# Optimization experiments

Measured on AMD Instinct MI355X. Metric: run time of the kernel, lower is better.

## Reference

```python
import jax, jax.numpy as jnp
import numpy as np

NUM_HEADS = 12
SIZE_PER_HEAD = 64
NEG_INF = -10000.0


def setup_inputs() -> dict:
    key = jax.random.key(0)
    k1, k2, k3, k4 = jax.random.split(key, 4)
    B, S, D = 2, 2048, 768
    x = jax.random.normal(k1, (B, S, D), dtype=jnp.float32)
    mask = jax.random.randint(k2, (B, S, S), 0, 2, dtype=jnp.int32)
    std = 0.02
    Wq = jax.random.normal(k3, (D, NUM_HEADS * SIZE_PER_HEAD), dtype=jnp.float32) * std
    Wk = jax.random.normal(k4, (D, NUM_HEADS * SIZE_PER_HEAD), dtype=jnp.float32) * std
    bq = jnp.zeros((NUM_HEADS * SIZE_PER_HEAD,), dtype=jnp.float32)
    bk = jnp.zeros((NUM_HEADS * SIZE_PER_HEAD,), dtype=jnp.float32)
    return {"x": x, "mask": mask, "Wq": Wq, "bq": bq, "Wk": Wk, "bk": bk}


def reference(x, mask, Wq, bq, Wk, bk):
    B, S, D = x.shape
    H, dh = NUM_HEADS, SIZE_PER_HEAD
    # Dense query/key projections (no activation), then split heads: [B,H,S,dh]
    q = (x @ Wq + bq).reshape(B, S, H, dh).transpose(0, 2, 1, 3)
    k = (x @ Wk + bk).reshape(B, S, H, dh).transpose(0, 2, 1, 3)
    # Scaled dot-product scores: [B,H,S,S]
    scores = jnp.einsum("bhqd,bhkd->bhqk", q, k) / jnp.sqrt(jnp.float32(dh))
    # Mask: [B,S,S] -> [B,1,S,S]; zeros get large negative additive bias
    adder = (1.0 - mask.astype(jnp.float32))[:, None, :, :] * NEG_INF
    probs = jax.nn.softmax(scores + adder, axis=-1)
    # dropout is identity at inference (training=None)
    return probs
```

## Files before the change

### kernel.cpp

```cpp
#include <hip/hip_runtime.h>
#include <stdint.h>

#define NUM_HEADS 12
#define DH 64
#define SEQ 2048
#define BATCH 2
#define DM 768
#define NQK 1536
#define LOG2E 1.44269504088896340736f

typedef short short8 __attribute__((ext_vector_type(8)));
typedef short short4_t __attribute__((ext_vector_type(4)));
typedef float f32x4 __attribute__((ext_vector_type(4)));

__device__ __forceinline__ short bf16_rne(float f) {
    union { float f; uint32_t u; } v; v.f = f;
    return (short)((v.u + 0x7FFFu + ((v.u >> 16) & 1u)) >> 16);
}

__global__ __launch_bounds__(256) void prep_kernel(const float* __restrict__ Wq,
                                                   const float* __restrict__ Wk,
                                                   const float* __restrict__ x,
                                                   const int* __restrict__ mask,
                                                   short* __restrict__ Wt,
                                                   short* __restrict__ Xb,
                                                   unsigned long long* __restrict__ Mb) {
    __shared__ float tile[32][33];
    const int bid = blockIdx.x;
    const int t = threadIdx.x;
    if (bid < 1152) {
        int n0 = (bid % 48) * 32;
        int k0 = (bid / 48) * 32;
        int tx = t & 31;
        int ty = t >> 5;
        const float* src = (n0 < DM) ? Wq : Wk;
        int nn0 = (n0 < DM) ? n0 : n0 - DM;
#pragma unroll
        for (int j = 0; j < 4; ++j) {
            int k = ty + 8 * j;
            tile[k][tx] = src[(size_t)(k0 + k) * DM + nn0 + tx];
        }
        __syncthreads();
#pragma unroll
        for (int j = 0; j < 4; ++j) {
            int n = ty + 8 * j;
            Wt[(size_t)(n0 + n) * DM + k0 + tx] = bf16_rne(tile[tx][n]);
        }
    } else if (bid < 1920) {
        size_t base = (size_t)(bid - 1152) * 4096;
#pragma unroll
        for (int j = 0; j < 4; ++j) {
            size_t i = base + (size_t)(t + j * 256) * 4;
            f32x4 v = *(const f32x4*)(x + i);
            short4_t s;
#pragma unroll
            for (int e = 0; e < 4; ++e) s[e] = bf16_rne(v[e]);
            *(short4_t*)(Xb + i) = s;
        }
    } else {
        int wid = (bid - 1920) * 4 + (t >> 6);
        int lane = t & 63;
        size_t base = (size_t)wid * 8;
#pragma unroll
        for (int i = 0; i < 8; ++i) {
            size_t w = base + i;
            int v = mask[w * 64 + lane];
            unsigned long long bal = __ballot(v != 0);
            if (lane == 0) Mb[w] = bal;
        }
    }
}

__global__ __launch_bounds__(256) void proj_kernel(const short* __restrict__ Xb,
                                                   const short* __restrict__ Wt,
                                                   const float* __restrict__ bq,
                                                   const float* __restrict__ bk,
                                                   short* __restrict__ QK) {
    __shared__ short As[128 * 72];
    __shared__ short Bs[128 * 72];
    const int m0 = blockIdx.x * 128;
    const int n0 = blockIdx.y * 128;
    const int t = threadIdx.x;
    const int lane = t & 63;
    const int w = t >> 6;
    const int wr = w >> 1, wc = w & 1;
    const int lr = lane & 15;
    const int lk = lane >> 4;

    f32x4 acc[4][4] = {};

    for (int k0 = 0; k0 < DM; k0 += 64) {
#pragma unroll
        for (int j = 0; j < 4; ++j) {
            int idx = t + 256 * j;
            int row = idx >> 3;
            int ch = idx & 7;
            *(short8*)&As[row * 72 + ch * 8] =
                *(const short8*)&Xb[(size_t)(m0 + row) * DM + k0 + ch * 8];
            *(short8*)&Bs[row * 72 + ch * 8] =
                *(const short8*)&Wt[(size_t)(n0 + row) * DM + k0 + ch * 8];
        }
        __syncthreads();
#pragma unroll
        for (int kk = 0; kk < 2; ++kk) {
            short8 a[4], bfr[4];
#pragma unroll
            for (int m = 0; m < 4; ++m)
                a[m] = *(short8*)&As[(wr * 64 + m * 16 + lr) * 72 + kk * 32 + lk * 8];
#pragma unroll
            for (int n = 0; n < 4; ++n)
                bfr[n] = *(short8*)&Bs[(wc * 64 + n * 16 + lr) * 72 + kk * 32 + lk * 8];
#pragma unroll
            for (int m = 0; m < 4; ++m)
#pragma unroll
                for (int n = 0; n < 4; ++n)
                    acc[m][n] = __builtin_amdgcn_mfma_f32_16x16x32_bf16(a[m], bfr[n], acc[m][n], 0, 0, 0);
        }
        __syncthreads();
    }

    const int orow = m0 + wr * 64;
    const int ocol = n0 + wc * 64;
#pragma unroll
    for (int m = 0; m < 4; ++m) {
#pragma unroll
        for (int n = 0; n < 4; ++n) {
            int col = ocol + n * 16 + lr;
            float bias = (col < DM) ? bq[col] : bk[col - DM];
            float scale = (col < DM) ? 0.125f * LOG2E : 1.0f;
#pragma unroll
            for (int r = 0; r < 4; ++r) {
                int row = orow + m * 16 + lk * 4 + r;
                QK[(size_t)row * NQK + col] = bf16_rne((acc[m][n][r] + bias) * scale);
            }
        }
    }
}

__global__ __launch_bounds__(256) void attn_kernel(const short* __restrict__ QK,
                                                   const unsigned long long* __restrict__ Mb,
                                                   float* __restrict__ out) {
    __shared__ short Ks[2][64 * 72];
    __shared__ float Pb[64 * 132];
    const int bid = blockIdx.x;
    const int xcd = bid & 7;
    const int jj = bid >> 3;
    const int bh = xcd * 3 + (jj >> 5);
    const int qblk = jj & 31;
    const int b = bh / NUM_HEADS;
    const int h = bh % NUM_HEADS;
    const int t = threadIdx.x;
    const int lane = t & 63;
    const int w = t >> 6;
    const int lr = lane & 15;
    const int lk = lane >> 4;
    const int wq = qblk * 64 + w * 16;

    short8 aq[2];
#pragma unroll
    for (int ks = 0; ks < 2; ++ks)
        aq[ks] = *(const short8*)&QK[(size_t)(b * SEQ + wq + lr) * NQK + h * DH + ks * 32 + lk * 8];

    float lrow[4] = {0.f, 0.f, 0.f, 0.f};
    const size_t mrow0 = (size_t)b * SEQ * (SEQ / 64);
    const int srow = t >> 3, sch = t & 7;

#define ATT_STAGE(KT)                                                                             \
    {                                                                                             \
        _Pragma("unroll") for (int tb = 0; tb < 2; ++tb) {                                        \
            *(short8*)&Ks[tb][srow * 72 + sch * 8] =                                              \
                *(const short8*)&QK[(size_t)(b * SEQ + (KT) + tb * 64 + srow) * NQK + DM +        \
                                    h * DH + sch * 8];                                            \
            *(short8*)&Ks[tb][(srow + 32) * 72 + sch * 8] =                                       \
                *(const short8*)&QK[(size_t)(b * SEQ + (KT) + tb * 64 + srow + 32) * NQK + DM +   \
                                    h * DH + sch * 8];                                            \
        }                                                                                         \
    }

    for (int kt = 0; kt < SEQ; kt += 128) {
        ATT_STAGE(kt)
        __syncthreads();
#pragma unroll
        for (int tb = 0; tb < 2; ++tb) {
            f32x4 sc[4];
#pragma unroll
            for (int nf = 0; nf < 4; ++nf) {
                short8 k0 = *(short8*)&Ks[tb][(nf * 16 + lr) * 72 + lk * 8];
                short8 k1 = *(short8*)&Ks[tb][(nf * 16 + lr) * 72 + 32 + lk * 8];
                f32x4 a = {0.f, 0.f, 0.f, 0.f};
                a = __builtin_amdgcn_mfma_f32_16x16x32_bf16(aq[0], k0, a, 0, 0, 0);
                a = __builtin_amdgcn_mfma_f32_16x16x32_bf16(aq[1], k1, a, 0, 0, 0);
                sc[nf] = a;
            }
#pragma unroll
            for (int r = 0; r < 4; ++r) {
                int q = wq + lk * 4 + r;
                unsigned long long mbs = Mb[mrow0 + (size_t)q * 32 + ((kt >> 6) + tb)] >> lr;
                float s = 0.f;
#pragma unroll
                for (int nf = 0; nf < 4; ++nf) {
                    float e = __builtin_amdgcn_exp2f(sc[nf][r]);
                    s += ((mbs >> (nf * 16)) & 1ull) ? e : 0.f;
                }
                lrow[r] += s;
            }
        }
        __syncthreads();
    }

    float inv[4];
#pragma unroll
    for (int r = 0; r < 4; ++r) {
        float l = lrow[r];
        l += __shfl_xor(l, 1, 64);
        l += __shfl_xor(l, 2, 64);
        l += __shfl_xor(l, 4, 64);
        l += __shfl_xor(l, 8, 64);
        inv[r] = 1.0f / l;
    }

    const size_t obase0 = ((size_t)((b * NUM_HEADS + h) * SEQ) + qblk * 64) * SEQ;
    for (int kt = 0; kt < SEQ; kt += 128) {
        ATT_STAGE(kt)
        __syncthreads();
#pragma unroll
        for (int tb = 0; tb < 2; ++tb) {
            f32x4 sc[4];
#pragma unroll
            for (int nf = 0; nf < 4; ++nf) {
                short8 k0 = *(short8*)&Ks[tb][(nf * 16 + lr) * 72 + lk * 8];
                short8 k1 = *(short8*)&Ks[tb][(nf * 16 + lr) * 72 + 32 + lk * 8];
                f32x4 a = {0.f, 0.f, 0.f, 0.f};
                a = __builtin_amdgcn_mfma_f32_16x16x32_bf16(aq[0], k0, a, 0, 0, 0);
                a = __builtin_amdgcn_mfma_f32_16x16x32_bf16(aq[1], k1, a, 0, 0, 0);
                sc[nf] = a;
            }
#pragma unroll
            for (int r = 0; r < 4; ++r) {
                int q = wq + lk * 4 + r;
                int qloc = w * 16 + lk * 4 + r;
                unsigned long long mbs = Mb[mrow0 + (size_t)q * 32 + ((kt >> 6) + tb)] >> lr;
#pragma unroll
                for (int nf = 0; nf < 4; ++nf) {
                    float p = __builtin_amdgcn_exp2f(sc[nf][r]) * inv[r];
                    Pb[qloc * 132 + tb * 64 + nf * 16 + lr] =
                        ((mbs >> (nf * 16)) & 1ull) ? p : 0.f;
                }
            }
        }
        __syncthreads();
#pragma unroll
        for (int g = 0; g < 8; ++g) {
            int row = g * 8 + (t >> 5);
            int col = (t & 31) * 4;
            *(f32x4*)&out[obase0 + (size_t)row * SEQ + kt + col] = *(f32x4*)&Pb[row * 132 + col];
        }
    }
#undef ATT_STAGE
}

extern "C" void kernel_launch(void* const* d_in, const int* in_sizes, int n_in,
                              void* d_out, int out_size, void* d_ws, size_t ws_size,
                              hipStream_t stream) {
    (void)in_sizes; (void)n_in; (void)out_size; (void)ws_size;
    const float* x = (const float*)d_in[0];
    const int* mask = (const int*)d_in[1];
    const float* Wq = (const float*)d_in[2];
    const float* bq = (const float*)d_in[3];
    const float* Wk = (const float*)d_in[4];
    const float* bk = (const float*)d_in[5];
    float* out = (float*)d_out;

    short* Wt = (short*)d_ws;
    short* Xb = Wt + (size_t)NQK * DM;
    short* QK = Xb + (size_t)BATCH * SEQ * DM;
    unsigned long long* Mb =
        (unsigned long long*)(QK + (size_t)BATCH * SEQ * NQK);

    prep_kernel<<<dim3(6016), 256, 0, stream>>>(Wq, Wk, x, mask, Wt, Xb, Mb);
    proj_kernel<<<dim3(BATCH * SEQ / 128, NQK / 128), 256, 0, stream>>>(Xb, Wt, bq, bk, QK);
    attn_kernel<<<dim3(768), 256, 0, stream>>>(QK, Mb, out);
}
```

Before: 156.7 us.

## Move mask packing into projection kernel and register-prefetch K tiles in attention

Mask bit-packing moves out of the prep kernel and into extra blocks of the projection GEMM launch, so the mask read runs alongside the GEMM instead of before it. Each of those blocks now packs 32 mask words per wave instead of 8. The attention kernel's two passes prefetch the next 128-key K tile into registers while computing on the current tile, then write it to shared memory after a barrier. This trades extra registers and an additional sync per iteration for hiding global load latency.

```diff
diff --git a/kernel.cpp b/kernel.cpp
--- a/kernel.cpp
+++ b/kernel.cpp
@@ -21,10 +21,8 @@
 __global__ __launch_bounds__(256) void prep_kernel(const float* __restrict__ Wq,
                                                    const float* __restrict__ Wk,
                                                    const float* __restrict__ x,
-                                                   const int* __restrict__ mask,
                                                    short* __restrict__ Wt,
-                                                   short* __restrict__ Xb,
-                                                   unsigned long long* __restrict__ Mb) {
+                                                   short* __restrict__ Xb) {
     __shared__ float tile[32][33];
     const int bid = blockIdx.x;
     const int t = threadIdx.x;
@@ -46,7 +44,7 @@
             int n = ty + 8 * j;
             Wt[(size_t)(n0 + n) * DM + k0 + tx] = bf16_rne(tile[tx][n]);
         }
-    } else if (bid < 1920) {
+    } else {
         size_t base = (size_t)(bid - 1152) * 4096;
 #pragma unroll
         for (int j = 0; j < 4; ++j) {
@@ -57,30 +55,34 @@
             for (int e = 0; e < 4; ++e) s[e] = bf16_rne(v[e]);
             *(short4_t*)(Xb + i) = s;
         }
-    } else {
-        int wid = (bid - 1920) * 4 + (t >> 6);
+    }
+}
+
+__global__ __launch_bounds__(256) void projm_kernel(const short* __restrict__ Xb,
+                                                    const short* __restrict__ Wt,
+                                                    const float* __restrict__ bq,
+                                                    const float* __restrict__ bk,
+                                                    const int* __restrict__ mask,
+                                                    short* __restrict__ QK,
+                                                    unsigned long long* __restrict__ Mb) {
+    __shared__ short As[128 * 72];
+    __shared__ short Bs[128 * 72];
+    const int bid = blockIdx.x;
+    const int t = threadIdx.x;
+    if (bid >= 384) {
+        int wid = (bid - 384) * 4 + (t >> 6);
         int lane = t & 63;
-        size_t base = (size_t)wid * 8;
-#pragma unroll
-        for (int i = 0; i < 8; ++i) {
+        size_t base = (size_t)wid * 32;
+        for (int i = 0; i < 32; ++i) {
             size_t w = base + i;
             int v = mask[w * 64 + lane];
             unsigned long long bal = __ballot(v != 0);
             if (lane == 0) Mb[w] = bal;
         }
-    }
-}
-
-__global__ __launch_bounds__(256) void proj_kernel(const short* __restrict__ Xb,
-                                                   const short* __restrict__ Wt,
-                                                   const float* __restrict__ bq,
-                                                   const float* __restrict__ bk,
-                                                   short* __restrict__ QK) {
-    __shared__ short As[128 * 72];
-    __shared__ short Bs[128 * 72];
-    const int m0 = blockIdx.x * 128;
-    const int n0 = blockIdx.y * 128;
-    const int t = threadIdx.x;
+        return;
+    }
+    const int m0 = (bid & 31) * 128;
+    const int n0 = (bid >> 5) * 128;
     const int lane = t & 63;
     const int w = t >> 6;
     const int wr = w >> 1, wc = w & 1;
@@ -164,22 +166,32 @@
     float lrow[4] = {0.f, 0.f, 0.f, 0.f};
     const size_t mrow0 = (size_t)b * SEQ * (SEQ / 64);
     const int srow = t >> 3, sch = t & 7;
-
-#define ATT_STAGE(KT)                                                                             \
-    {                                                                                             \
-        _Pragma("unroll") for (int tb = 0; tb < 2; ++tb) {                                        \
-            *(short8*)&Ks[tb][srow * 72 + sch * 8] =                                              \
-                *(const short8*)&QK[(size_t)(b * SEQ + (KT) + tb * 64 + srow) * NQK + DM +        \
-                                    h * DH + sch * 8];                                            \
-            *(short8*)&Ks[tb][(srow + 32) * 72 + sch * 8] =                                       \
-                *(const short8*)&QK[(size_t)(b * SEQ + (KT) + tb * 64 + srow + 32) * NQK + DM +   \
-                                    h * DH + sch * 8];                                            \
-        }                                                                                         \
-    }
-
-    for (int kt = 0; kt < SEQ; kt += 128) {
-        ATT_STAGE(kt)
-        __syncthreads();
+    short8 rs0, rs1, rs2, rs3;
+
+#define ATT_LOAD(KT)                                                                         \
+    {                                                                                        \
+        const short* kp =                                                                    \
+            &QK[(size_t)(b * SEQ + (KT) + srow) * NQK + DM + h * DH + sch * 8];              \
+        rs0 = *(const short8*)kp;                                                            \
+        rs1 = *(const short8*)(kp + (size_t)32 * NQK);                                       \
+        rs2 = *(const short8*)(kp + (size_t)64 * NQK);                                       \
+        rs3 = *(const short8*)(kp + (size_t)96 * NQK);                                       \
+    }
+
+#define ATT_WRITE()                                                                          \
+    {                                                                                        \
+        *(short8*)&Ks[0][srow * 72 + sch * 8] = rs0;                                         \
+        *(short8*)&Ks[0][(srow + 32) * 72 + sch * 8] = rs1;                                  \
+        *(short8*)&Ks[1][srow * 72 + sch * 8] = rs2;                                         \
+        *(short8*)&Ks[1][(srow + 32) * 72 + sch * 8] = rs3;                                  \
+    }
+
+    ATT_LOAD(0)
+    ATT_WRITE()
+    __syncthreads();
+    for (int g = 0; g < 16; ++g) {
+        const int kt = g * 128;
+        if (g < 15) ATT_LOAD(kt + 128)
 #pragma unroll
         for (int tb = 0; tb < 2; ++tb) {
             f32x4 sc[4];
@@ -206,6 +218,10 @@
             }
         }
         __syncthreads();
+        if (g < 15) {
+            ATT_WRITE()
+        }
+        __syncthreads();
     }
 
     float inv[4];
@@ -220,9 +236,12 @@
     }
 
     const size_t obase0 = ((size_t)((b * NUM_HEADS + h) * SEQ) + qblk * 64) * SEQ;
-    for (int kt = 0; kt < SEQ; kt += 128) {
-        ATT_STAGE(kt)
-        __syncthreads();
+    ATT_LOAD(0)
+    ATT_WRITE()
+    __syncthreads();
+    for (int g = 0; g < 16; ++g) {
+        const int kt = g * 128;
+        if (g < 15) ATT_LOAD(kt + 128)
 #pragma unroll
         for (int tb = 0; tb < 2; ++tb) {
             f32x4 sc[4];
@@ -250,13 +269,18 @@
         }
         __syncthreads();
 #pragma unroll
-        for (int g = 0; g < 8; ++g) {
-            int row = g * 8 + (t >> 5);
+        for (int gg = 0; gg < 8; ++gg) {
+            int row = gg * 8 + (t >> 5);
             int col = (t & 31) * 4;
             *(f32x4*)&out[obase0 + (size_t)row * SEQ + kt + col] = *(f32x4*)&Pb[row * 132 + col];
         }
-    }
-#undef ATT_STAGE
+        if (g < 15) {
+            ATT_WRITE()
+        }
+        __syncthreads();
+    }
+#undef ATT_LOAD
+#undef ATT_WRITE
 }
 
 extern "C" void kernel_launch(void* const* d_in, const int* in_sizes, int n_in,
@@ -277,7 +301,7 @@
     unsigned long long* Mb =
         (unsigned long long*)(QK + (size_t)BATCH * SEQ * NQK);
 
-    prep_kernel<<<dim3(6016), 256, 0, stream>>>(Wq, Wk, x, mask, Wt, Xb, Mb);
-    proj_kernel<<<dim3(BATCH * SEQ / 128, NQK / 128), 256, 0, stream>>>(Xb, Wt, bq, bk, QK);
+    prep_kernel<<<dim3(1920), 256, 0, stream>>>(Wq, Wk, x, Wt, Xb);
+    projm_kernel<<<dim3(1408), 256, 0, stream>>>(Xb, Wt, bq, bk, mask, QK, Mb);
     attn_kernel<<<dim3(768), 256, 0, stream>>>(QK, Mb, out);
 }
```

Result: slower. 167.0 us (+6.6%).
